# Optimization experiments

Hardware: AMD Instinct MI355X
Metric: run time of the kernel (lower is better)

Reference implementation:

```python
import jax, jax.numpy as jnp
import numpy as np

DIM = 512
HEADS = 8
LF, P = 32, 32
N = LF * P
LOC_DIM = 64  # loc_emd_dim == locf_dim == 64
SCALE = (DIM // HEADS) ** -0.5


def _position_matrix(boxes):
    # boxes: [N,4] x1y1x2y2 -> [N,N,4] relative geometry (relation-network style)
    x1, y1, x2, y2 = jnp.split(boxes, 4, axis=1)  # each [N,1]
    w = x2 - x1 + 1.0
    h = y2 - y1 + 1.0
    cx = 0.5 * (x1 + x2)
    cy = 0.5 * (y1 + y2)
    dx = jnp.log(jnp.maximum(jnp.abs((cx - cx.T) / w), 1e-3))
    dy = jnp.log(jnp.maximum(jnp.abs((cy - cy.T) / h), 1e-3))
    dw = jnp.log(w.T / w)
    dh = jnp.log(h.T / h)
    return jnp.stack([dx, dy, dw, dh], axis=-1)  # [N,N,4]


def _position_embedding(pos_mat, feat_dim=LOC_DIM, wave_length=1000.0):
    # pos_mat: [N,N,4] -> [N,N,feat_dim] sin/cos embedding
    nf = feat_dim // 8
    dim_mat = wave_length ** (jnp.arange(nf, dtype=jnp.float32) * (8.0 / feat_dim))  # [nf]
    div = pos_mat[..., None] * 100.0 / dim_mat  # [N,N,4,nf]
    emb = jnp.concatenate([jnp.sin(div), jnp.cos(div)], axis=-1)  # [N,N,4,2nf]
    return emb.reshape(pos_mat.shape[0], pos_mat.shape[1], feat_dim)


def setup_inputs() -> dict:
    key = jax.random.key(0)
    ks = jax.random.split(key, 8)
    x = jax.random.normal(ks[0], (1, N, DIM), jnp.float32)
    x_reg = jax.random.normal(ks[1], (1, N, DIM), jnp.float32)
    # valid boxes: x1y1x2y2 within a ~1000x600 frame
    cx = jax.random.uniform(ks[2], (LF, P, 1)) * 1000.0
    cy = jax.random.uniform(ks[3], (LF, P, 1)) * 600.0
    w = jax.random.uniform(ks[4], (LF, P, 1)) * 150.0 + 10.0
    h = jax.random.uniform(ks[5], (LF, P, 1)) * 150.0 + 10.0
    locs = jnp.concatenate([cx - w / 2, cy - h / 2, cx + w / 2, cy + h / 2], axis=-1)
    W_qkv = jax.random.normal(ks[6], (3 * DIM, DIM), jnp.float32) * 0.02
    W_loc = jax.random.normal(ks[7], (HEADS, LOC_DIM), jnp.float32) * 0.01  # 1x1 conv weight
    b_loc = jnp.zeros((HEADS,), jnp.float32)
    return {"x": x, "x_reg": x_reg, "locs": locs, "W_qkv": W_qkv, "W_loc": W_loc, "b_loc": b_loc}


def reference(x, x_reg, locs, W_qkv, W_loc, b_loc):
    B, n, C = x.shape
    boxes = locs.reshape(-1, 4)
    # location embedding -> 1x1 conv -> ReLU  (attn_lt: [H,N,N])
    pos_emb = _position_embedding(_position_matrix(boxes), LOC_DIM)  # [N,N,64]
    attn_lt = jax.nn.relu(jnp.einsum('nmf,hf->hnm', pos_emb, W_loc) + b_loc[:, None, None])
    # qkv projection (bias=False)
    qkv = (x @ W_qkv.T).reshape(B, n, 3, HEADS, C // HEADS)
    qkv = jnp.transpose(qkv, (2, 0, 3, 1, 4))  # [3,B,H,N,hd]
    q, k, v = qkv[0], qkv[1], qkv[2]
    attn = jnp.einsum('bhnd,bhmd->bhnm', q, k) * SCALE
    attn = attn + jnp.log(attn_lt + 1e-6)[None]  # loc_fuse_type == 'add'
    attn = jax.nn.softmax(attn, axis=-1)
    out = jnp.einsum('bhnm,bhmd->bhnd', attn, v)
    return jnp.transpose(out, (0, 2, 1, 3)).reshape(B, n, C)
```

## Files before the change

### kernel.cpp

```cpp
#include <hip/hip_runtime.h>
#include <hip/hip_bf16.h>


namespace {
constexpr int NN   = 1024;
constexpr int CDIM = 512;
constexpr int NH   = 8;
constexpr int HD   = 64;
constexpr int NOUT = 3 * CDIM;
constexpr int PROJ_BLOCKS = (NN / 64) * (NOUT / 64);
constexpr float QSCALE = 0.125f;

constexpr size_t QKBF_OFF_U16 = 0;
constexpr size_t VT_OFF_U16   = (size_t)2 * NH * NN * HD;
constexpr size_t XB_OFF_U16   = VT_OFF_U16 + (size_t)NH * HD * NN;
constexpr size_t WB_OFF_U16   = XB_OFF_U16 + (size_t)NN * CDIM;
constexpr size_t L_OFF_U16    = WB_OFF_U16 + (size_t)NOUT * CDIM;
constexpr size_t END_U16      = L_OFF_U16 + (size_t)NH * NN * NN;
constexpr size_t BF_OFF_F32   = END_U16 / 2;
constexpr size_t WR_OFF_F32   = BF_OFF_F32 + 6 * NN;
}

typedef __attribute__((ext_vector_type(8))) short short8v;
typedef __attribute__((ext_vector_type(4))) float f32x4;
typedef __attribute__((ext_vector_type(2))) float f32x2;

__device__ __forceinline__ unsigned short f2bf(float f) {
  union { float f; unsigned int u; } v; v.f = f;
  unsigned int u = v.u;
  u += 0x7fffu + ((u >> 16) & 1u);
  return (unsigned short)(u >> 16);
}
__device__ __forceinline__ float b2f(unsigned short u) {
  union { unsigned int u; float f; } v; v.u = ((unsigned int)u) << 16; return v.f;
}

__global__ __launch_bounds__(256) void k_cvt(const float* __restrict__ x,
                                             const float* __restrict__ wq,
                                             const float* __restrict__ locs,
                                             const float* __restrict__ wloc,
                                             const float* __restrict__ bloc,
                                             unsigned short* __restrict__ xb,
                                             unsigned short* __restrict__ wb,
                                             float* __restrict__ bf,
                                             float* __restrict__ wr) {
  constexpr int XTOT = NN * CDIM;
  constexpr int CVT_BLOCKS = 1280;
  int b = blockIdx.x;
  int tid = threadIdx.x;
  if (b < CVT_BLOCKS) {
    int idx = (b * 256 + tid) * 4;
    if (idx < XTOT) {
      float4 v = *reinterpret_cast<const float4*>(x + idx);
      ushort4 o;
      o.x = f2bf(v.x); o.y = f2bf(v.y); o.z = f2bf(v.z); o.w = f2bf(v.w);
      *reinterpret_cast<ushort4*>(xb + idx) = o;
    } else {
      int j = idx - XTOT;
      float4 v = *reinterpret_cast<const float4*>(wq + j);
      ushort4 o;
      o.x = f2bf(v.x); o.y = f2bf(v.y); o.z = f2bf(v.z); o.w = f2bf(v.w);
      *reinterpret_cast<ushort4*>(wb + j) = o;
    }
  } else {
    for (int i = tid; i < NN; i += 256) {
      float4 b4 = reinterpret_cast<const float4*>(locs)[i];
      float x1 = b4.x, y1 = b4.y, x2 = b4.z, y2 = b4.w;
      float w = x2 - x1 + 1.0f;
      float h = y2 - y1 + 1.0f;
      bf[0 * NN + i] = 0.5f * (x1 + x2);
      bf[1 * NN + i] = 0.5f * (y1 + y2);
      bf[2 * NN + i] = w;
      bf[3 * NN + i] = h;
      bf[4 * NN + i] = logf(w);
      bf[5 * NN + i] = logf(h);
    }
    for (int i = tid; i < 512; i += 256) {
      int hh = i & 7, c = (i >> 3) & 1, j = (i >> 4) & 3, t = i >> 6;
      wr[i] = wloc[hh * 64 + j * 16 + c * 8 + t];
    }
    if (tid < 8) wr[512 + tid] = bloc[tid];
  }
}

__global__ __launch_bounds__(256) void k_mid(const unsigned short* __restrict__ xb,
                                             const unsigned short* __restrict__ wb,
                                             unsigned short* __restrict__ qk_bf,
                                             unsigned short* __restrict__ vt,
                                             const float* __restrict__ bf,
                                             const float* __restrict__ wr,
                                             unsigned short* __restrict__ L) {
  __shared__ unsigned short A_lds[64][72];
  __shared__ unsigned short B_lds[64][72];
  int blk = blockIdx.x;
  int tid = threadIdx.x;

  if (blk >= PROJ_BLOCKS) {
    int blk2 = blk - PROJ_BLOCKS;
    int n = blk2 >> 2;
    int m = (blk2 & 3) * 256 + tid;
    const float* cx = bf;
    const float* cy = bf + NN;
    const float* bw = bf + 2 * NN;
    const float* bh = bf + 3 * NN;
    const float* lw = bf + 4 * NN;
    const float* lh = bf + 5 * NN;

    float cxn = cx[n], cyn = cy[n], wn = bw[n], hn = bh[n], lwn = lw[n], lhn = lh[n];
    float dx = __logf(fmaxf(fabsf((cxn - cx[m]) / wn), 1e-3f));
    float dy = __logf(fmaxf(fabsf((cyn - cy[m]) / hn), 1e-3f));
    float dw = lw[m] - lwn;
    float dh = lh[m] - lhn;
    float pos[4] = {dx, dy, dw, dh};

    const float ANG[8] = {100.0f, 42.169650342858224f, 17.78279410038923f,
                          7.498942093324559f, 3.1622776601683795f, 1.333521432163324f,
                          0.5623413251903491f, 0.23713737056616552f};

    f32x2 acc2[4] = {(f32x2){0.f, 0.f}, (f32x2){0.f, 0.f},
                     (f32x2){0.f, 0.f}, (f32x2){0.f, 0.f}};
#pragma unroll
    for (int t = 0; t < 8; ++t) {
#pragma unroll
      for (int j = 0; j < 4; ++j) {
        float s, c;
        __sincosf(pos[j] * ANG[t], &s, &c);
        const f32x2* wp2 = reinterpret_cast<const f32x2*>(wr + (t * 4 + j) * 16);
        f32x2 s2 = {s, s}, c2 = {c, c};
#pragma unroll
        for (int i = 0; i < 4; ++i) {
          acc2[i] += s2 * wp2[i] + c2 * wp2[4 + i];
        }
      }
    }
#pragma unroll
    for (int hh = 0; hh < 8; ++hh) {
      float v = fmaxf(acc2[hh >> 1][hh & 1] + wr[512 + hh], 0.0f);
      L[((size_t)hh * NN + n) * NN + m] = f2bf(v + 1e-6f);
    }
  } else {
    int t = blk;
    int n0 = (t & 15) * 64, i0 = (t >> 4) * 64;
    int w = tid >> 6, l = tid & 63, g = l >> 4, c = l & 15;
    int sr = tid >> 2;
    int sc = (tid & 3) * 16;

    f32x4 acc[4];
#pragma unroll
    for (int ct = 0; ct < 4; ++ct) acc[ct] = (f32x4){0.f, 0.f, 0.f, 0.f};

    for (int kt = 0; kt < CDIM; kt += 64) {
      const unsigned short* asrc = xb + (size_t)(n0 + sr) * CDIM + kt + sc;
      const unsigned short* bsrc = wb + (size_t)(i0 + sr) * CDIM + kt + sc;
      *reinterpret_cast<short8v*>(&A_lds[sr][sc])     = *reinterpret_cast<const short8v*>(asrc);
      *reinterpret_cast<short8v*>(&A_lds[sr][sc + 8]) = *reinterpret_cast<const short8v*>(asrc + 8);
      *reinterpret_cast<short8v*>(&B_lds[sr][sc])     = *reinterpret_cast<const short8v*>(bsrc);
      *reinterpret_cast<short8v*>(&B_lds[sr][sc + 8]) = *reinterpret_cast<const short8v*>(bsrc + 8);
      __syncthreads();
#pragma unroll
      for (int kks = 0; kks < 2; ++kks) {
        short8v a = *reinterpret_cast<const short8v*>(&A_lds[16 * w + c][kks * 32 + 8 * g]);
#pragma unroll
        for (int ct = 0; ct < 4; ++ct) {
          short8v b = *reinterpret_cast<const short8v*>(&B_lds[16 * ct + c][kks * 32 + 8 * g]);
          acc[ct] = __builtin_amdgcn_mfma_f32_16x16x32_bf16(a, b, acc[ct], 0, 0, 0);
        }
      }
      __syncthreads();
    }

    int s = i0 >> 9;
    int hh = (i0 >> 6) & 7;
    if (s < 2) {
      float scale = (s == 0) ? QSCALE : 1.0f;
      unsigned short* dst = qk_bf + ((size_t)(s * NH + hh) * NN) * HD;
#pragma unroll
      for (int ct = 0; ct < 4; ++ct)
#pragma unroll
        for (int r = 0; r < 4; ++r) {
          int n = n0 + 16 * w + 4 * g + r;
          dst[(size_t)n * HD + 16 * ct + c] = f2bf(acc[ct][r] * scale);
        }
    } else {
#pragma unroll
      for (int ct = 0; ct < 4; ++ct)
#pragma unroll
        for (int r = 0; r < 4; ++r) {
          A_lds[16 * w + 4 * g + r][16 * ct + c] = f2bf(acc[ct][r]);
        }
      __syncthreads();
      int d = tid >> 2;
      int nn0 = (tid & 3) * 16;
      unsigned short o[16];
#pragma unroll
      for (int nn = 0; nn < 16; ++nn) o[nn] = A_lds[nn0 + nn][d];
      unsigned short* dst = vt + ((size_t)hh * HD + d) * NN + n0 + nn0;
      *reinterpret_cast<short8v*>(dst)     = *reinterpret_cast<short8v*>(&o[0]);
      *reinterpret_cast<short8v*>(dst + 8) = *reinterpret_cast<short8v*>(&o[8]);
    }
  }
}

__global__ __launch_bounds__(512) void k_mha(const unsigned short* __restrict__ qk,
                                             const unsigned short* __restrict__ vt,
                                             const unsigned short* __restrict__ L,
                                             float* __restrict__ out) {
  __shared__ short8v smem16[3200];
  auto V = reinterpret_cast<unsigned short(*)[64][40]>(smem16);
  auto P = reinterpret_cast<unsigned short(*)[640]>(
      reinterpret_cast<char*>(smem16) + 40960);
  auto accs = reinterpret_cast<float(*)[16][68]>(smem16);
  auto mls = reinterpret_cast<float(*)[2][16]>(reinterpret_cast<char*>(smem16) + 34816);

  int tid = threadIdx.x;
  int w = tid >> 6;
  int l = tid & 63;
  int g = l >> 4;
  int c = l & 15;
  int h = blockIdx.y;
  int n0 = blockIdx.x * 16;

  const unsigned short* qb = qk + ((size_t)(0 * NH + h) * NN + n0) * HD;
  const unsigned short* kb = qk + ((size_t)(1 * NH + h) * NN) * HD;
  const unsigned short* vb = vt + (size_t)h * HD * NN;
  const unsigned short* Lb = L + ((size_t)h * NN + n0 + 4 * g) * NN;

  short8v a_lo = *reinterpret_cast<const short8v*>(qb + (size_t)c * HD + 8 * g);
  short8v a_hi = *reinterpret_cast<const short8v*>(qb + (size_t)c * HD + 32 + 8 * g);

  f32x4 acc[4];
#pragma unroll
  for (int ct = 0; ct < 4; ++ct) acc[ct] = (f32x4){0.f, 0.f, 0.f, 0.f};
  float m_run[4] = {-3.0e38f, -3.0e38f, -3.0e38f, -3.0e38f};
  float l_run[4] = {0.f, 0.f, 0.f, 0.f};

#pragma unroll
  for (int it = 0; it < 4; ++it) {
    int mt = w * 128 + it * 32;

#pragma unroll
    for (int p = 0; p < 4; ++p) {
      int d = p * 16 + (l >> 2);
      int key16 = (l & 3) * 8;
      *reinterpret_cast<short8v*>(&V[w][d][key16]) =
          *reinterpret_cast<const short8v*>(vb + (size_t)d * NN + mt + key16);
    }

    float t0[4], t1[4];
#pragma unroll
    for (int r = 0; r < 4; ++r) {
      t0[r] = b2f(Lb[(size_t)r * NN + mt + c]);
      t1[r] = b2f(Lb[(size_t)r * NN + mt + 16 + c]);
    }

    const unsigned short* k0p = kb + (size_t)(mt + c) * HD + 8 * g;
    const unsigned short* k1p = kb + (size_t)(mt + 16 + c) * HD + 8 * g;
    short8v b0_lo = *reinterpret_cast<const short8v*>(k0p);
    short8v b0_hi = *reinterpret_cast<const short8v*>(k0p + 32);
    short8v b1_lo = *reinterpret_cast<const short8v*>(k1p);
    short8v b1_hi = *reinterpret_cast<const short8v*>(k1p + 32);

    __builtin_amdgcn_s_setprio(1);
    f32x4 z = {0.f, 0.f, 0.f, 0.f};
    f32x4 s0 = __builtin_amdgcn_mfma_f32_16x16x32_bf16(a_lo, b0_lo, z, 0, 0, 0);
    s0 = __builtin_amdgcn_mfma_f32_16x16x32_bf16(a_hi, b0_hi, s0, 0, 0, 0);
    f32x4 s1 = __builtin_amdgcn_mfma_f32_16x16x32_bf16(a_lo, b1_lo, z, 0, 0, 0);
    s1 = __builtin_amdgcn_mfma_f32_16x16x32_bf16(a_hi, b1_hi, s1, 0, 0, 0);
    __builtin_amdgcn_s_setprio(0);

    float sc[4], p0[4], p1[4];
#pragma unroll
    for (int r = 0; r < 4; ++r) {
      float mx = fmaxf(s0[r], s1[r]);
      mx = fmaxf(mx, __shfl_xor(mx, 1));
      mx = fmaxf(mx, __shfl_xor(mx, 2));
      mx = fmaxf(mx, __shfl_xor(mx, 4));
      mx = fmaxf(mx, __shfl_xor(mx, 8));
      float m_new = fmaxf(m_run[r], mx);
      sc[r] = __expf(m_run[r] - m_new);
      p0[r] = t0[r] * __expf(s0[r] - m_new);
      p1[r] = t1[r] * __expf(s1[r] - m_new);
      float ps = p0[r] + p1[r];
      ps += __shfl_xor(ps, 1);
      ps += __shfl_xor(ps, 2);
      ps += __shfl_xor(ps, 4);
      ps += __shfl_xor(ps, 8);
      l_run[r] = l_run[r] * sc[r] + ps;
      m_run[r] = m_new;
    }
#pragma unroll
    for (int ct = 0; ct < 4; ++ct)
#pragma unroll
      for (int r = 0; r < 4; ++r) acc[ct][r] *= sc[r];

#pragma unroll
    for (int r = 0; r < 4; ++r) {
      P[w][(4 * g + r) * 40 + c] = f2bf(p0[r]);
      P[w][(4 * g + r) * 40 + 16 + c] = f2bf(p1[r]);
    }
    __builtin_amdgcn_wave_barrier();

    short8v pa = *reinterpret_cast<const short8v*>(&P[w][c * 40 + 8 * g]);
    __builtin_amdgcn_s_setprio(1);
#pragma unroll
    for (int ct = 0; ct < 4; ++ct) {
      short8v vbf = *reinterpret_cast<const short8v*>(&V[w][ct * 16 + c][8 * g]);
      acc[ct] = __builtin_amdgcn_mfma_f32_16x16x32_bf16(pa, vbf, acc[ct], 0, 0, 0);
    }
    __builtin_amdgcn_s_setprio(0);
    __builtin_amdgcn_wave_barrier();
  }

  __syncthreads();

  if (c == 0) {
#pragma unroll
    for (int r = 0; r < 4; ++r) {
      mls[w][0][4 * g + r] = m_run[r];
      mls[w][1][4 * g + r] = l_run[r];
    }
  }
#pragma unroll
  for (int ct = 0; ct < 4; ++ct)
#pragma unroll
    for (int r = 0; r < 4; ++r) accs[w][4 * g + r][ct * 16 + c] = acc[ct][r];
  __syncthreads();

#pragma unroll
  for (int o = tid; o < 16 * 64; o += 512) {
    int row = o >> 6, col = o & 63;
    float mfin = mls[0][0][row];
#pragma unroll
    for (int w2i = 1; w2i < 8; ++w2i) mfin = fmaxf(mfin, mls[w2i][0][row]);
    float lfin = 0.f, val = 0.f;
#pragma unroll
    for (int w2i = 0; w2i < 8; ++w2i) {
      float scw = __expf(mls[w2i][0][row] - mfin);
      lfin += mls[w2i][1][row] * scw;
      val += accs[w2i][row][col] * scw;
    }
    out[(size_t)(n0 + row) * CDIM + h * HD + col] = val / lfin;
  }
}

extern "C" void kernel_launch(void* const* d_in, const int* in_sizes, int n_in,
                              void* d_out, int out_size, void* d_ws, size_t ws_size,
                              hipStream_t stream) {
  const float* x    = (const float*)d_in[0];
  const float* locs = (const float*)d_in[2];
  const float* wqkv = (const float*)d_in[3];
  const float* wloc = (const float*)d_in[4];
  const float* bloc = (const float*)d_in[5];
  float* out = (float*)d_out;
  float* ws = (float*)d_ws;
  unsigned short* ws_u16 = (unsigned short*)d_ws;

  unsigned short* qk_bf = ws_u16 + QKBF_OFF_U16;
  unsigned short* vt_bf = ws_u16 + VT_OFF_U16;
  unsigned short* xb    = ws_u16 + XB_OFF_U16;
  unsigned short* wb    = ws_u16 + WB_OFF_U16;
  unsigned short* L     = ws_u16 + L_OFF_U16;
  float* bf = ws + BF_OFF_F32;
  float* wr = ws + WR_OFF_F32;

  k_cvt<<<dim3(1281), dim3(256), 0, stream>>>(x, wqkv, locs, wloc, bloc, xb, wb, bf, wr);
  k_mid<<<dim3(PROJ_BLOCKS + 4096), dim3(256), 0, stream>>>(
      xb, wb, qk_bf, vt_bf, bf, wr, L);
  k_mha<<<dim3(NN / 16, NH), dim3(512), 0, stream>>>(qk_bf, vt_bf, L, out);
}
```

Measured before the change: 52.51 us.

## Precompute per-box sin/cos tables and defer softmax row-sum reductions

The dw/dh sin/cos terms are now built from per-box tables using angle-difference identities. k_cvt computes those tables once, so k_mid evaluates only 16 sincos per pair instead of 32 and adds table loads and multiplies. In k_mha the per-iteration cross-lane reduction of the softmax row sum is moved out of the loop to a single reduction at the end. The final merge now computes per-row scale factors once in shared memory instead of repeating them for every output element. Accuracy may shift slightly because the angle identities use fast sincos on larger arguments.

```diff
diff --git a/kernel.cpp b/kernel.cpp
--- a/kernel.cpp
+++ b/kernel.cpp
@@ -19,6 +19,7 @@
 constexpr size_t END_U16      = L_OFF_U16 + (size_t)NH * NN * NN;
 constexpr size_t BF_OFF_F32   = END_U16 / 2;
 constexpr size_t WR_OFF_F32   = BF_OFF_F32 + 6 * NN;
+constexpr size_t TB_OFF_F32   = WR_OFF_F32 + 544;
 }
 
 typedef __attribute__((ext_vector_type(8))) short short8v;
@@ -43,7 +44,8 @@
                                              unsigned short* __restrict__ xb,
                                              unsigned short* __restrict__ wb,
                                              float* __restrict__ bf,
-                                             float* __restrict__ wr) {
+                                             float* __restrict__ wr,
+                                             float* __restrict__ tb) {
   constexpr int XTOT = NN * CDIM;
   constexpr int CVT_BLOCKS = 1280;
   int b = blockIdx.x;
@@ -63,6 +65,9 @@
       *reinterpret_cast<ushort4*>(wb + j) = o;
     }
   } else {
+    const float ANG[8] = {100.0f, 42.169650342858224f, 17.78279410038923f,
+                          7.498942093324559f, 3.1622776601683795f, 1.333521432163324f,
+                          0.5623413251903491f, 0.23713737056616552f};
     for (int i = tid; i < NN; i += 256) {
       float4 b4 = reinterpret_cast<const float4*>(locs)[i];
       float x1 = b4.x, y1 = b4.y, x2 = b4.z, y2 = b4.w;
@@ -72,8 +77,18 @@
       bf[1 * NN + i] = 0.5f * (y1 + y2);
       bf[2 * NN + i] = w;
       bf[3 * NN + i] = h;
-      bf[4 * NN + i] = logf(w);
-      bf[5 * NN + i] = logf(h);
+      float lwv = logf(w);
+      float lhv = logf(h);
+#pragma unroll
+      for (int t = 0; t < 8; ++t) {
+        float s, c;
+        __sincosf(lwv * ANG[t], &s, &c);
+        tb[(size_t)(t * 4 + 0) * NN + i] = s;
+        tb[(size_t)(t * 4 + 1) * NN + i] = c;
+        __sincosf(lhv * ANG[t], &s, &c);
+        tb[(size_t)(t * 4 + 2) * NN + i] = s;
+        tb[(size_t)(t * 4 + 3) * NN + i] = c;
+      }
     }
     for (int i = tid; i < 512; i += 256) {
       int hh = i & 7, c = (i >> 3) & 1, j = (i >> 4) & 3, t = i >> 6;
@@ -89,6 +104,7 @@
                                              unsigned short* __restrict__ vt,
                                              const float* __restrict__ bf,
                                              const float* __restrict__ wr,
+                                             const float* __restrict__ tb,
                                              unsigned short* __restrict__ L) {
   __shared__ unsigned short A_lds[64][72];
   __shared__ unsigned short B_lds[64][72];
@@ -103,30 +119,37 @@
     const float* cy = bf + NN;
     const float* bw = bf + 2 * NN;
     const float* bh = bf + 3 * NN;
-    const float* lw = bf + 4 * NN;
-    const float* lh = bf + 5 * NN;
-
-    float cxn = cx[n], cyn = cy[n], wn = bw[n], hn = bh[n], lwn = lw[n], lhn = lh[n];
+
+    float cxn = cx[n], cyn = cy[n], wn = bw[n], hn = bh[n];
     float dx = __logf(fmaxf(fabsf((cxn - cx[m]) / wn), 1e-3f));
     float dy = __logf(fmaxf(fabsf((cyn - cy[m]) / hn), 1e-3f));
-    float dw = lw[m] - lwn;
-    float dh = lh[m] - lhn;
-    float pos[4] = {dx, dy, dw, dh};
 
     const float ANG[8] = {100.0f, 42.169650342858224f, 17.78279410038923f,
                           7.498942093324559f, 3.1622776601683795f, 1.333521432163324f,
                           0.5623413251903491f, 0.23713737056616552f};
 
+    const float* tm = tb + m;
+    const float* tn = tb + n;
+
     f32x2 acc2[4] = {(f32x2){0.f, 0.f}, (f32x2){0.f, 0.f},
                      (f32x2){0.f, 0.f}, (f32x2){0.f, 0.f}};
 #pragma unroll
     for (int t = 0; t < 8; ++t) {
+      float sj[4], cj[4];
+      __sincosf(dx * ANG[t], &sj[0], &cj[0]);
+      __sincosf(dy * ANG[t], &sj[1], &cj[1]);
+      float swm = tm[(size_t)(t * 4 + 0) * NN], cwm = tm[(size_t)(t * 4 + 1) * NN];
+      float shm = tm[(size_t)(t * 4 + 2) * NN], chm = tm[(size_t)(t * 4 + 3) * NN];
+      float swn = tn[(size_t)(t * 4 + 0) * NN], cwn = tn[(size_t)(t * 4 + 1) * NN];
+      float shn = tn[(size_t)(t * 4 + 2) * NN], chn = tn[(size_t)(t * 4 + 3) * NN];
+      sj[2] = swm * cwn - cwm * swn;
+      cj[2] = cwm * cwn + swm * swn;
+      sj[3] = shm * chn - chm * shn;
+      cj[3] = chm * chn + shm * shn;
 #pragma unroll
       for (int j = 0; j < 4; ++j) {
-        float s, c;
-        __sincosf(pos[j] * ANG[t], &s, &c);
         const f32x2* wp2 = reinterpret_cast<const f32x2*>(wr + (t * 4 + j) * 16);
-        f32x2 s2 = {s, s}, c2 = {c, c};
+        f32x2 s2 = {sj[j], sj[j]}, c2 = {cj[j], cj[j]};
 #pragma unroll
         for (int i = 0; i < 4; ++i) {
           acc2[i] += s2 * wp2[i] + c2 * wp2[4 + i];
@@ -211,6 +234,8 @@
       reinterpret_cast<char*>(smem16) + 40960);
   auto accs = reinterpret_cast<float(*)[16][68]>(smem16);
   auto mls = reinterpret_cast<float(*)[2][16]>(reinterpret_cast<char*>(smem16) + 34816);
+  auto scw2 = reinterpret_cast<float(*)[16]>(reinterpret_cast<char*>(smem16) + 35840);
+  auto rlf = reinterpret_cast<float*>(reinterpret_cast<char*>(smem16) + 36352);
 
   int tid = threadIdx.x;
   int w = tid >> 6;
@@ -280,12 +305,7 @@
       sc[r] = __expf(m_run[r] - m_new);
       p0[r] = t0[r] * __expf(s0[r] - m_new);
       p1[r] = t1[r] * __expf(s1[r] - m_new);
-      float ps = p0[r] + p1[r];
-      ps += __shfl_xor(ps, 1);
-      ps += __shfl_xor(ps, 2);
-      ps += __shfl_xor(ps, 4);
-      ps += __shfl_xor(ps, 8);
-      l_run[r] = l_run[r] * sc[r] + ps;
+      l_run[r] = l_run[r] * sc[r] + (p0[r] + p1[r]);
       m_run[r] = m_new;
     }
 #pragma unroll
@@ -311,6 +331,16 @@
     __builtin_amdgcn_wave_barrier();
   }
 
+#pragma unroll
+  for (int r = 0; r < 4; ++r) {
+    float ls = l_run[r];
+    ls += __shfl_xor(ls, 1);
+    ls += __shfl_xor(ls, 2);
+    ls += __shfl_xor(ls, 4);
+    ls += __shfl_xor(ls, 8);
+    l_run[r] = ls;
+  }
+
   __syncthreads();
 
   if (c == 0) {
@@ -326,20 +356,31 @@
     for (int r = 0; r < 4; ++r) accs[w][4 * g + r][ct * 16 + c] = acc[ct][r];
   __syncthreads();
 
+  if (tid < 16) {
+    int row = tid;
+    float mfin = mls[0][0][row];
+#pragma unroll
+    for (int w2i = 1; w2i < 8; ++w2i) mfin = fmaxf(mfin, mls[w2i][0][row]);
+    float lfin = 0.f;
+#pragma unroll
+    for (int w2i = 0; w2i < 8; ++w2i) {
+      float scv = __expf(mls[w2i][0][row] - mfin);
+      scw2[w2i][row] = scv;
+      lfin += mls[w2i][1][row] * scv;
+    }
+    rlf[row] = 1.0f / lfin;
+  }
+  __syncthreads();
+
 #pragma unroll
   for (int o = tid; o < 16 * 64; o += 512) {
     int row = o >> 6, col = o & 63;
-    float mfin = mls[0][0][row];
-#pragma unroll
-    for (int w2i = 1; w2i < 8; ++w2i) mfin = fmaxf(mfin, mls[w2i][0][row]);
-    float lfin = 0.f, val = 0.f;
+    float val = 0.f;
 #pragma unroll
     for (int w2i = 0; w2i < 8; ++w2i) {
-      float scw = __expf(mls[w2i][0][row] - mfin);
-      lfin += mls[w2i][1][row] * scw;
-      val += accs[w2i][row][col] * scw;
-    }
-    out[(size_t)(n0 + row) * CDIM + h * HD + col] = val / lfin;
+      val += scw2[w2i][row] * accs[w2i][row][col];
+    }
+    out[(size_t)(n0 + row) * CDIM + h * HD + col] = val * rlf[row];
   }
 }
 
@@ -362,9 +403,10 @@
   unsigned short* L     = ws_u16 + L_OFF_U16;
   float* bf = ws + BF_OFF_F32;
   float* wr = ws + WR_OFF_F32;
-
-  k_cvt<<<dim3(1281), dim3(256), 0, stream>>>(x, wqkv, locs, wloc, bloc, xb, wb, bf, wr);
+  float* tb = ws + TB_OFF_F32;
+
+  k_cvt<<<dim3(1281), dim3(256), 0, stream>>>(x, wqkv, locs, wloc, bloc, xb, wb, bf, wr, tb);
   k_mid<<<dim3(PROJ_BLOCKS + 4096), dim3(256), 0, stream>>>(
-      xb, wb, qk_bf, vt_bf, bf, wr, L);
+      xb, wb, qk_bf, vt_bf, bf, wr, tb, L);
   k_mha<<<dim3(NN / 16, NH), dim3(512), 0, stream>>>(qk_bf, vt_bf, L, out);
 }
```

After: 54.44 us. 1.04x slower.

## Fuse fp32-to-bf16 conversion into projection GEMM and defer softmax row-sum reduction

Applied to the files above, without the earlier changes.

The separate conversion pass over x and W_qkv is removed. The projection GEMM now loads fp32 directly and converts to bf16 while staging tiles into LDS, and the prep kernel shrinks to box features and weight reordering. This drops a full write and re-read of the bf16 copies and shortens the prep kernel, but the GEMM now reads twice as many global bytes per tile, and each x and W tile is converted many times. In the attention kernel, the per-iteration cross-lane sum of probabilities is deferred to a single reduction after the loop, and the final merge precomputes per-row scale factors and reciprocals once instead of per output element.

```diff
diff --git a/kernel.cpp b/kernel.cpp
--- a/kernel.cpp
+++ b/kernel.cpp
@@ -34,47 +34,35 @@
 __device__ __forceinline__ float b2f(unsigned short u) {
   union { unsigned int u; float f; } v; v.u = ((unsigned int)u) << 16; return v.f;
 }
-
-__global__ __launch_bounds__(256) void k_cvt(const float* __restrict__ x,
-                                             const float* __restrict__ wq,
-                                             const float* __restrict__ locs,
-                                             const float* __restrict__ wloc,
-                                             const float* __restrict__ bloc,
-                                             unsigned short* __restrict__ xb,
-                                             unsigned short* __restrict__ wb,
-                                             float* __restrict__ bf,
-                                             float* __restrict__ wr) {
-  constexpr int XTOT = NN * CDIM;
-  constexpr int CVT_BLOCKS = 1280;
+__device__ __forceinline__ short8v cvt8(float4 a, float4 b) {
+  short8v o;
+  o[0] = (short)f2bf(a.x); o[1] = (short)f2bf(a.y);
+  o[2] = (short)f2bf(a.z); o[3] = (short)f2bf(a.w);
+  o[4] = (short)f2bf(b.x); o[5] = (short)f2bf(b.y);
+  o[6] = (short)f2bf(b.z); o[7] = (short)f2bf(b.w);
+  return o;
+}
+
+__global__ __launch_bounds__(256) void k_prep(const float* __restrict__ locs,
+                                              const float* __restrict__ wloc,
+                                              const float* __restrict__ bloc,
+                                              float* __restrict__ bf,
+                                              float* __restrict__ wr) {
   int b = blockIdx.x;
   int tid = threadIdx.x;
-  if (b < CVT_BLOCKS) {
-    int idx = (b * 256 + tid) * 4;
-    if (idx < XTOT) {
-      float4 v = *reinterpret_cast<const float4*>(x + idx);
-      ushort4 o;
-      o.x = f2bf(v.x); o.y = f2bf(v.y); o.z = f2bf(v.z); o.w = f2bf(v.w);
-      *reinterpret_cast<ushort4*>(xb + idx) = o;
-    } else {
-      int j = idx - XTOT;
-      float4 v = *reinterpret_cast<const float4*>(wq + j);
-      ushort4 o;
-      o.x = f2bf(v.x); o.y = f2bf(v.y); o.z = f2bf(v.z); o.w = f2bf(v.w);
-      *reinterpret_cast<ushort4*>(wb + j) = o;
-    }
+  if (b < 4) {
+    int i = b * 256 + tid;
+    float4 b4 = reinterpret_cast<const float4*>(locs)[i];
+    float x1 = b4.x, y1 = b4.y, x2 = b4.z, y2 = b4.w;
+    float w = x2 - x1 + 1.0f;
+    float h = y2 - y1 + 1.0f;
+    bf[0 * NN + i] = 0.5f * (x1 + x2);
+    bf[1 * NN + i] = 0.5f * (y1 + y2);
+    bf[2 * NN + i] = w;
+    bf[3 * NN + i] = h;
+    bf[4 * NN + i] = logf(w);
+    bf[5 * NN + i] = logf(h);
   } else {
-    for (int i = tid; i < NN; i += 256) {
-      float4 b4 = reinterpret_cast<const float4*>(locs)[i];
-      float x1 = b4.x, y1 = b4.y, x2 = b4.z, y2 = b4.w;
-      float w = x2 - x1 + 1.0f;
-      float h = y2 - y1 + 1.0f;
-      bf[0 * NN + i] = 0.5f * (x1 + x2);
-      bf[1 * NN + i] = 0.5f * (y1 + y2);
-      bf[2 * NN + i] = w;
-      bf[3 * NN + i] = h;
-      bf[4 * NN + i] = logf(w);
-      bf[5 * NN + i] = logf(h);
-    }
     for (int i = tid; i < 512; i += 256) {
       int hh = i & 7, c = (i >> 3) & 1, j = (i >> 4) & 3, t = i >> 6;
       wr[i] = wloc[hh * 64 + j * 16 + c * 8 + t];
@@ -83,8 +71,8 @@
   }
 }
 
-__global__ __launch_bounds__(256) void k_mid(const unsigned short* __restrict__ xb,
-                                             const unsigned short* __restrict__ wb,
+__global__ __launch_bounds__(256) void k_mid(const float* __restrict__ x,
+                                             const float* __restrict__ wq,
                                              unsigned short* __restrict__ qk_bf,
                                              unsigned short* __restrict__ vt,
                                              const float* __restrict__ bf,
@@ -150,12 +138,16 @@
     for (int ct = 0; ct < 4; ++ct) acc[ct] = (f32x4){0.f, 0.f, 0.f, 0.f};
 
     for (int kt = 0; kt < CDIM; kt += 64) {
-      const unsigned short* asrc = xb + (size_t)(n0 + sr) * CDIM + kt + sc;
-      const unsigned short* bsrc = wb + (size_t)(i0 + sr) * CDIM + kt + sc;
-      *reinterpret_cast<short8v*>(&A_lds[sr][sc])     = *reinterpret_cast<const short8v*>(asrc);
-      *reinterpret_cast<short8v*>(&A_lds[sr][sc + 8]) = *reinterpret_cast<const short8v*>(asrc + 8);
-      *reinterpret_cast<short8v*>(&B_lds[sr][sc])     = *reinterpret_cast<const short8v*>(bsrc);
-      *reinterpret_cast<short8v*>(&B_lds[sr][sc + 8]) = *reinterpret_cast<const short8v*>(bsrc + 8);
+      const float4* af = reinterpret_cast<const float4*>(
+          x + (size_t)(n0 + sr) * CDIM + kt + sc);
+      const float4* bq = reinterpret_cast<const float4*>(
+          wq + (size_t)(i0 + sr) * CDIM + kt + sc);
+      float4 a0 = af[0], a1 = af[1], a2 = af[2], a3 = af[3];
+      float4 b0 = bq[0], b1 = bq[1], b2 = bq[2], b3 = bq[3];
+      *reinterpret_cast<short8v*>(&A_lds[sr][sc])     = cvt8(a0, a1);
+      *reinterpret_cast<short8v*>(&A_lds[sr][sc + 8]) = cvt8(a2, a3);
+      *reinterpret_cast<short8v*>(&B_lds[sr][sc])     = cvt8(b0, b1);
+      *reinterpret_cast<short8v*>(&B_lds[sr][sc + 8]) = cvt8(b2, b3);
       __syncthreads();
 #pragma unroll
       for (int kks = 0; kks < 2; ++kks) {
@@ -211,6 +203,8 @@
       reinterpret_cast<char*>(smem16) + 40960);
   auto accs = reinterpret_cast<float(*)[16][68]>(smem16);
   auto mls = reinterpret_cast<float(*)[2][16]>(reinterpret_cast<char*>(smem16) + 34816);
+  auto scw2 = reinterpret_cast<float(*)[16]>(reinterpret_cast<char*>(smem16) + 35840);
+  auto rlf = reinterpret_cast<float*>(reinterpret_cast<char*>(smem16) + 36352);
 
   int tid = threadIdx.x;
   int w = tid >> 6;
@@ -280,12 +274,7 @@
       sc[r] = __expf(m_run[r] - m_new);
       p0[r] = t0[r] * __expf(s0[r] - m_new);
       p1[r] = t1[r] * __expf(s1[r] - m_new);
-      float ps = p0[r] + p1[r];
-      ps += __shfl_xor(ps, 1);
-      ps += __shfl_xor(ps, 2);
-      ps += __shfl_xor(ps, 4);
-      ps += __shfl_xor(ps, 8);
-      l_run[r] = l_run[r] * sc[r] + ps;
+      l_run[r] = l_run[r] * sc[r] + (p0[r] + p1[r]);
       m_run[r] = m_new;
     }
 #pragma unroll
@@ -311,6 +300,16 @@
     __builtin_amdgcn_wave_barrier();
   }
 
+#pragma unroll
+  for (int r = 0; r < 4; ++r) {
+    float ls = l_run[r];
+    ls += __shfl_xor(ls, 1);
+    ls += __shfl_xor(ls, 2);
+    ls += __shfl_xor(ls, 4);
+    ls += __shfl_xor(ls, 8);
+    l_run[r] = ls;
+  }
+
   __syncthreads();
 
   if (c == 0) {
@@ -326,20 +325,31 @@
     for (int r = 0; r < 4; ++r) accs[w][4 * g + r][ct * 16 + c] = acc[ct][r];
   __syncthreads();
 
+  if (tid < 16) {
+    int row = tid;
+    float mfin = mls[0][0][row];
+#pragma unroll
+    for (int w2i = 1; w2i < 8; ++w2i) mfin = fmaxf(mfin, mls[w2i][0][row]);
+    float lfin = 0.f;
+#pragma unroll
+    for (int w2i = 0; w2i < 8; ++w2i) {
+      float scv = __expf(mls[w2i][0][row] - mfin);
+      scw2[w2i][row] = scv;
+      lfin += mls[w2i][1][row] * scv;
+    }
+    rlf[row] = 1.0f / lfin;
+  }
+  __syncthreads();
+
 #pragma unroll
   for (int o = tid; o < 16 * 64; o += 512) {
     int row = o >> 6, col = o & 63;
-    float mfin = mls[0][0][row];
-#pragma unroll
-    for (int w2i = 1; w2i < 8; ++w2i) mfin = fmaxf(mfin, mls[w2i][0][row]);
-    float lfin = 0.f, val = 0.f;
+    float val = 0.f;
 #pragma unroll
     for (int w2i = 0; w2i < 8; ++w2i) {
-      float scw = __expf(mls[w2i][0][row] - mfin);
-      lfin += mls[w2i][1][row] * scw;
-      val += accs[w2i][row][col] * scw;
-    }
-    out[(size_t)(n0 + row) * CDIM + h * HD + col] = val / lfin;
+      val += scw2[w2i][row] * accs[w2i][row][col];
+    }
+    out[(size_t)(n0 + row) * CDIM + h * HD + col] = val * rlf[row];
   }
 }
 
@@ -357,14 +367,12 @@
 
   unsigned short* qk_bf = ws_u16 + QKBF_OFF_U16;
   unsigned short* vt_bf = ws_u16 + VT_OFF_U16;
-  unsigned short* xb    = ws_u16 + XB_OFF_U16;
-  unsigned short* wb    = ws_u16 + WB_OFF_U16;
   unsigned short* L     = ws_u16 + L_OFF_U16;
   float* bf = ws + BF_OFF_F32;
   float* wr = ws + WR_OFF_F32;
 
-  k_cvt<<<dim3(1281), dim3(256), 0, stream>>>(x, wqkv, locs, wloc, bloc, xb, wb, bf, wr);
+  k_prep<<<dim3(5), dim3(256), 0, stream>>>(locs, wloc, bloc, bf, wr);
   k_mid<<<dim3(PROJ_BLOCKS + 4096), dim3(256), 0, stream>>>(
-      xb, wb, qk_bf, vt_bf, bf, wr, L);
+      x, wqkv, qk_bf, vt_bf, bf, wr, L);
   k_mha<<<dim3(NN / 16, NH), dim3(512), 0, stream>>>(qk_bf, vt_bf, L, out);
 }
```

After: 55.36 us. 5.4% more time.
